# Kernel tuning notes

Measured on AMD Instinct MI355X. Metric: run time of the kernel, lower is better.

The kernel has to match this reference:

```python
import jax, jax.numpy as jnp
import numpy as np

V, H, B, T = 100000, 512, 4096, 524288
EPS = 1e-5

def setup_inputs() -> dict:
    key = jax.random.key(0)
    ks = jax.random.split(key, 8)
    tokens = jax.random.randint(ks[0], (T,), 0, V, dtype=jnp.int32)
    seg_ids = jnp.sort(jax.random.randint(ks[1], (T,), 0, B, dtype=jnp.int32))
    t = jax.random.bernoulli(ks[2], 0.5, (B,)).astype(jnp.float32)
    emb = jax.random.normal(ks[3], (V, H), dtype=jnp.float32) * 0.1
    W1 = jax.random.normal(ks[4], (H, H), dtype=jnp.float32) * (1.0 / np.sqrt(H))
    b1 = jnp.zeros((H,), jnp.float32)
    gamma = jnp.ones((H,), jnp.float32)
    beta = jnp.zeros((H,), jnp.float32)
    w2 = jax.random.normal(ks[5], (H,), dtype=jnp.float32) * (1.0 / np.sqrt(H))
    b2 = jnp.zeros((), jnp.float32)
    return {"tokens": tokens, "seg_ids": seg_ids, "t": t, "emb": emb,
            "W1": W1, "b1": b1, "gamma": gamma, "beta": beta, "w2": w2, "b2": b2}

def reference(tokens, seg_ids, t, emb, W1, b1, gamma, beta, w2, b2):
    nb = t.shape[0]
    # fused gather + segment-mean (bag-of-words), replaces the per-sample loop
    gathered = emb[tokens]  # [T, H]
    sums = jax.ops.segment_sum(gathered, seg_ids, num_segments=nb)  # [B, H]
    counts = jax.ops.segment_sum(jnp.ones((tokens.shape[0],), jnp.float32), seg_ids, num_segments=nb)
    bow = sums / jnp.maximum(counts, 1.0)[:, None]  # [B, H]
    # Linear -> BatchNorm1d (training-mode batch stats, biased var) -> ReLU
    z = bow @ W1.T + b1  # [B, H]
    mu = jnp.mean(z, axis=0)
    var = jnp.mean((z - mu) ** 2, axis=0)
    zn = (z - mu) * jax.lax.rsqrt(var + EPS) * gamma + beta
    h = jax.nn.relu(zn)  # dropout treated as identity (eval mode) for determinism
    logits = h @ w2 + b2  # [B]
    # BCEWithLogitsLoss: mean(softplus(logit) - t*logit), numerically stable
    loss = jnp.mean(jnp.logaddexp(0.0, logits) - t * logits)
    return (loss, logits)
```

## Files before the change

kernel.cpp:

```cpp
#include <hip/hip_runtime.h>
#include <hip/hip_bf16.h>
#include <hip/hip_fp16.h>
#include <math.h>

constexpr int NTOK = 524288;
constexpr int NB   = 4096;
constexpr int H    = 512;
constexpr float EPS = 1e-5f;

typedef _Float16 half8 __attribute__((ext_vector_type(8)));
typedef float f32x4 __attribute__((ext_vector_type(4)));
struct h4 { __half2 a, b; };

__global__ __launch_bounds__(256) void k_convert(
    const float* __restrict__ src, h4* __restrict__ dst) {
  size_t i = (size_t)blockIdx.x * 256 + threadIdx.x;
  float4 v = ((const float4*)src)[i];
  h4 o;
  o.a = __floats2half2_rn(v.x, v.y);
  o.b = __floats2half2_rn(v.z, v.w);
  dst[i] = o;
}

__global__ __launch_bounds__(256) void k_gather_mean(
    const int* __restrict__ tokens, const int* __restrict__ seg,
    const half8* __restrict__ embh, half8* __restrict__ bow_h) {
  const int b = blockIdx.x;
  int lo = 0, hi = NTOK;
  while (lo < hi) { int mid = (lo + hi) >> 1; if (seg[mid] < b) lo = mid + 1; else hi = mid; }
  const int start = lo;
  hi = NTOK;
  while (lo < hi) { int mid = (lo + hi) >> 1; if (seg[mid] < b + 1) lo = mid + 1; else hi = mid; }
  const int end = lo;

  const int tid = threadIdx.x;
  const int lane = tid & 63;
  const int g = tid >> 6;

  float acc[8] = {};
  int i = start + g;
  for (; i + 12 < end; i += 16) {
    half8 v0 = embh[(size_t)tokens[i]      * 64 + lane];
    half8 v1 = embh[(size_t)tokens[i + 4]  * 64 + lane];
    half8 v2 = embh[(size_t)tokens[i + 8]  * 64 + lane];
    half8 v3 = embh[(size_t)tokens[i + 12] * 64 + lane];
#pragma unroll
    for (int j = 0; j < 8; ++j)
      acc[j] += (float)v0[j] + (float)v1[j] + (float)v2[j] + (float)v3[j];
  }
  for (; i < end; i += 4) {
    half8 v0 = embh[(size_t)tokens[i] * 64 + lane];
#pragma unroll
    for (int j = 0; j < 8; ++j) acc[j] += (float)v0[j];
  }

  __shared__ float part[3][64][9];
  if (g > 0) {
#pragma unroll
    for (int j = 0; j < 8; ++j) part[g - 1][lane][j] = acc[j];
  }
  __syncthreads();
  if (g == 0) {
    const int cnt = end - start;
    const float s = 1.0f / (float)(cnt > 0 ? cnt : 1);
    half8 o;
#pragma unroll
    for (int j = 0; j < 8; ++j) {
      float v = acc[j] + part[0][lane][j] + part[1][lane][j] + part[2][lane][j];
      o[j] = (_Float16)(v * s);
    }
    bow_h[(size_t)b * 64 + lane] = o;
  }
}

__global__ __launch_bounds__(256) void k_gemm_mfma(
    const _Float16* __restrict__ A,
    const _Float16* __restrict__ Bw,
    const float* __restrict__ b1, float* __restrict__ C) {
  const int tid = threadIdx.x;
  const int lane = tid & 63;
  const int gw = blockIdx.x * 4 + (tid >> 6);
  const int m0 = (gw >> 3) * 16;
  const int n0 = (gw & 7) * 64;
  const int l15 = lane & 15, quad = lane >> 4;

  f32x4 acc0 = {}, acc1 = {}, acc2 = {}, acc3 = {};
  const _Float16* ap = A + (size_t)(m0 + l15) * H + quad * 8;
  const _Float16* bp = Bw + (size_t)(n0 + l15) * H + quad * 8;

#pragma unroll
  for (int k = 0; k < H; k += 32) {
    half8 af  = *(const half8*)(ap + k);
    half8 bf0 = *(const half8*)(bp + k);
    half8 bf1 = *(const half8*)(bp + 16 * H + k);
    half8 bf2 = *(const half8*)(bp + 32 * H + k);
    half8 bf3 = *(const half8*)(bp + 48 * H + k);
    acc0 = __builtin_amdgcn_mfma_f32_16x16x32_f16(af, bf0, acc0, 0, 0, 0);
    acc1 = __builtin_amdgcn_mfma_f32_16x16x32_f16(af, bf1, acc1, 0, 0, 0);
    acc2 = __builtin_amdgcn_mfma_f32_16x16x32_f16(af, bf2, acc2, 0, 0, 0);
    acc3 = __builtin_amdgcn_mfma_f32_16x16x32_f16(af, bf3, acc3, 0, 0, 0);
  }

  const float bn0v = b1[n0 + l15];
  const float bn1v = b1[n0 + 16 + l15];
  const float bn2v = b1[n0 + 32 + l15];
  const float bn3v = b1[n0 + 48 + l15];
  float* crow = C + (size_t)(m0 + quad * 4) * H + n0 + l15;
#pragma unroll
  for (int r = 0; r < 4; ++r) {
    crow[(size_t)r * H]      = acc0[r] + bn0v;
    crow[(size_t)r * H + 16] = acc1[r] + bn1v;
    crow[(size_t)r * H + 32] = acc2[r] + bn2v;
    crow[(size_t)r * H + 48] = acc3[r] + bn3v;
  }
}

__global__ __launch_bounds__(256) void k_colstats(
    const float* __restrict__ z, float* __restrict__ ps, float* __restrict__ pss) {
  const int blk = blockIdx.x;
  const int c0 = threadIdx.x * 2;
  const int r0 = blk * 64;
  float s0 = 0, s1 = 0, q0 = 0, q1 = 0;
  for (int r = 0; r < 64; ++r) {
    float2 v = *(const float2*)&z[(size_t)(r0 + r) * H + c0];
    s0 += v.x; s1 += v.y;
    q0 += v.x * v.x; q1 += v.y * v.y;
  }
  ps[blk * H + c0] = s0; ps[blk * H + c0 + 1] = s1;
  pss[blk * H + c0] = q0; pss[blk * H + c0 + 1] = q1;
}

__global__ __launch_bounds__(128) void k_finalize(
    const float* __restrict__ ps, const float* __restrict__ pss,
    const float* __restrict__ gamma, const float* __restrict__ beta,
    float* __restrict__ scale, float* __restrict__ shift) {
  const int c = blockIdx.x * 128 + threadIdx.x;
  float s = 0, q = 0;
#pragma unroll 8
  for (int i = 0; i < 64; ++i) { s += ps[i * H + c]; q += pss[i * H + c]; }
  const float mu = s * (1.0f / NB);
  const float var = q * (1.0f / NB) - mu * mu;
  const float rstd = rsqrtf(var + EPS);
  const float sc = rstd * gamma[c];
  scale[c] = sc;
  shift[c] = beta[c] - mu * sc;
}

__global__ __launch_bounds__(256) void k_bn_dot(
    const float* __restrict__ z, const float* __restrict__ scale,
    const float* __restrict__ shift, const float* __restrict__ w2,
    const float* __restrict__ b2, float* __restrict__ out) {
  const int tid = threadIdx.x;
  const int wave = tid >> 6, lane = tid & 63;
  const int b = blockIdx.x * 4 + wave;
  const float4* __restrict__ z4 = (const float4*)(z + (size_t)b * H);
  const float4* __restrict__ sc4 = (const float4*)scale;
  const float4* __restrict__ sh4 = (const float4*)shift;
  const float4* __restrict__ w24 = (const float4*)w2;
  float acc = 0.f;
#pragma unroll
  for (int i = lane; i < 128; i += 64) {
    float4 zv = z4[i], sc = sc4[i], sh = sh4[i], w = w24[i];
    float h0 = fmaxf(zv.x * sc.x + sh.x, 0.f);
    float h1 = fmaxf(zv.y * sc.y + sh.y, 0.f);
    float h2 = fmaxf(zv.z * sc.z + sh.z, 0.f);
    float h3 = fmaxf(zv.w * sc.w + sh.w, 0.f);
    acc += h0 * w.x + h1 * w.y + h2 * w.z + h3 * w.w;
  }
#pragma unroll
  for (int off = 32; off > 0; off >>= 1) acc += __shfl_down(acc, off, 64);
  if (lane == 0) out[1 + b] = acc + b2[0];
}

__global__ __launch_bounds__(1024) void k_loss(
    const float* __restrict__ t, float* __restrict__ d_out) {
  const int tid = threadIdx.x;
  float s = 0.f;
#pragma unroll
  for (int b = tid; b < NB; b += 1024) {
    float x = d_out[1 + b];
    float sp = fmaxf(x, 0.f) + log1pf(expf(-fabsf(x)));
    s += sp - t[b] * x;
  }
  __shared__ float red[1024];
  red[tid] = s;
  __syncthreads();
  for (int off = 512; off > 0; off >>= 1) {
    if (tid < off) red[tid] += red[tid + off];
    __syncthreads();
  }
  if (tid == 0) d_out[0] = red[0] * (1.0f / NB);
}

extern "C" void kernel_launch(void* const* d_in, const int* in_sizes, int n_in,
                              void* d_out, int out_size, void* d_ws, size_t ws_size,
                              hipStream_t stream) {
  const int*   tokens = (const int*)d_in[0];
  const int*   seg    = (const int*)d_in[1];
  const float* t      = (const float*)d_in[2];
  const float* emb    = (const float*)d_in[3];
  const float* W1     = (const float*)d_in[4];
  const float* b1     = (const float*)d_in[5];
  const float* gamma  = (const float*)d_in[6];
  const float* beta   = (const float*)d_in[7];
  const float* w2     = (const float*)d_in[8];
  const float* b2     = (const float*)d_in[9];
  float* out = (float*)d_out;

  char* wsb = (char*)d_ws;
  half8*    embh  = (half8*)wsb;
  _Float16* W1h   = (_Float16*)(wsb + 102400000);
  half8*    bow_h = (half8*)(wsb + 102924288);
  float*    z     = (float*)(wsb + 107118592);
  float*    ps    = (float*)(wsb + 115507200);
  float*    pss   = ps + 64 * H;
  float*    scale = pss + 64 * H;
  float*    shift = scale + H;

  k_convert<<<50000, 256, 0, stream>>>(emb, (h4*)embh);
  k_convert<<<256, 256, 0, stream>>>(W1, (h4*)W1h);
  k_gather_mean<<<NB, 256, 0, stream>>>(tokens, seg, embh, bow_h);
  k_gemm_mfma<<<512, 256, 0, stream>>>((const _Float16*)bow_h, W1h, b1, z);
  k_colstats<<<64, 256, 0, stream>>>(z, ps, pss);
  k_finalize<<<4, 128, 0, stream>>>(ps, pss, gamma, beta, scale, shift);
  k_bn_dot<<<NB / 4, 256, 0, stream>>>(z, scale, shift, w2, b2, out);
  k_loss<<<1, 1024, 0, stream>>>(t, out);
}
```

Before: 420.3 us.

## Precompute segment bounds, unroll gather deeper, fuse loss into BN-dot kernel

```diff
diff --git a/kernel.cpp b/kernel.cpp
--- a/kernel.cpp
+++ b/kernel.cpp
@@ -11,6 +11,17 @@
 typedef _Float16 half8 __attribute__((ext_vector_type(8)));
 typedef float f32x4 __attribute__((ext_vector_type(4)));
 struct h4 { __half2 a, b; };
+
+__global__ __launch_bounds__(256) void k_seg_bounds(
+    const int* __restrict__ seg, int* __restrict__ bounds) {
+  const int i = blockIdx.x * 256 + threadIdx.x;
+  const int s = seg[i];
+  const int sp = (i == 0) ? -1 : seg[i - 1];
+  for (int b = sp + 1; b <= s; ++b) bounds[b] = i;
+  if (i == NTOK - 1) {
+    for (int b = s + 1; b <= NB; ++b) bounds[b] = NTOK;
+  }
+}
 
 __global__ __launch_bounds__(256) void k_convert(
     const float* __restrict__ src, h4* __restrict__ dst) {
@@ -23,15 +34,11 @@
 }
 
 __global__ __launch_bounds__(256) void k_gather_mean(
-    const int* __restrict__ tokens, const int* __restrict__ seg,
+    const int* __restrict__ tokens, const int* __restrict__ bounds,
     const half8* __restrict__ embh, half8* __restrict__ bow_h) {
   const int b = blockIdx.x;
-  int lo = 0, hi = NTOK;
-  while (lo < hi) { int mid = (lo + hi) >> 1; if (seg[mid] < b) lo = mid + 1; else hi = mid; }
-  const int start = lo;
-  hi = NTOK;
-  while (lo < hi) { int mid = (lo + hi) >> 1; if (seg[mid] < b + 1) lo = mid + 1; else hi = mid; }
-  const int end = lo;
+  const int start = bounds[b];
+  const int end   = bounds[b + 1];
 
   const int tid = threadIdx.x;
   const int lane = tid & 63;
@@ -39,14 +46,19 @@
 
   float acc[8] = {};
   int i = start + g;
-  for (; i + 12 < end; i += 16) {
+  for (; i + 28 < end; i += 32) {
     half8 v0 = embh[(size_t)tokens[i]      * 64 + lane];
     half8 v1 = embh[(size_t)tokens[i + 4]  * 64 + lane];
     half8 v2 = embh[(size_t)tokens[i + 8]  * 64 + lane];
     half8 v3 = embh[(size_t)tokens[i + 12] * 64 + lane];
+    half8 v4 = embh[(size_t)tokens[i + 16] * 64 + lane];
+    half8 v5 = embh[(size_t)tokens[i + 20] * 64 + lane];
+    half8 v6 = embh[(size_t)tokens[i + 24] * 64 + lane];
+    half8 v7 = embh[(size_t)tokens[i + 28] * 64 + lane];
 #pragma unroll
     for (int j = 0; j < 8; ++j)
-      acc[j] += (float)v0[j] + (float)v1[j] + (float)v2[j] + (float)v3[j];
+      acc[j] += ((float)v0[j] + (float)v1[j]) + ((float)v2[j] + (float)v3[j]) +
+                ((float)v4[j] + (float)v5[j]) + ((float)v6[j] + (float)v7[j]);
   }
   for (; i < end; i += 4) {
     half8 v0 = embh[(size_t)tokens[i] * 64 + lane];
@@ -133,8 +145,10 @@
 __global__ __launch_bounds__(128) void k_finalize(
     const float* __restrict__ ps, const float* __restrict__ pss,
     const float* __restrict__ gamma, const float* __restrict__ beta,
-    float* __restrict__ scale, float* __restrict__ shift) {
+    float* __restrict__ scale, float* __restrict__ shift,
+    float* __restrict__ d_out) {
   const int c = blockIdx.x * 128 + threadIdx.x;
+  if (c == 0) d_out[0] = 0.f;
   float s = 0, q = 0;
 #pragma unroll 8
   for (int i = 0; i < 64; ++i) { s += ps[i * H + c]; q += pss[i * H + c]; }
@@ -146,10 +160,11 @@
   shift[c] = beta[c] - mu * sc;
 }
 
-__global__ __launch_bounds__(256) void k_bn_dot(
+__global__ __launch_bounds__(256) void k_bn_dot_loss(
     const float* __restrict__ z, const float* __restrict__ scale,
     const float* __restrict__ shift, const float* __restrict__ w2,
-    const float* __restrict__ b2, float* __restrict__ out) {
+    const float* __restrict__ b2, const float* __restrict__ t,
+    float* __restrict__ out) {
   const int tid = threadIdx.x;
   const int wave = tid >> 6, lane = tid & 63;
   const int b = blockIdx.x * 4 + wave;
@@ -169,27 +184,19 @@
   }
 #pragma unroll
   for (int off = 32; off > 0; off >>= 1) acc += __shfl_down(acc, off, 64);
-  if (lane == 0) out[1 + b] = acc + b2[0];
-}
-
-__global__ __launch_bounds__(1024) void k_loss(
-    const float* __restrict__ t, float* __restrict__ d_out) {
-  const int tid = threadIdx.x;
-  float s = 0.f;
-#pragma unroll
-  for (int b = tid; b < NB; b += 1024) {
-    float x = d_out[1 + b];
-    float sp = fmaxf(x, 0.f) + log1pf(expf(-fabsf(x)));
-    s += sp - t[b] * x;
-  }
-  __shared__ float red[1024];
-  red[tid] = s;
+
+  __shared__ float lred[4];
+  if (lane == 0) {
+    const float x = acc + b2[0];
+    out[1 + b] = x;
+    const float sp = fmaxf(x, 0.f) + log1pf(expf(-fabsf(x)));
+    lred[wave] = sp - t[b] * x;
+  }
   __syncthreads();
-  for (int off = 512; off > 0; off >>= 1) {
-    if (tid < off) red[tid] += red[tid + off];
-    __syncthreads();
-  }
-  if (tid == 0) d_out[0] = red[0] * (1.0f / NB);
+  if (tid == 0) {
+    const float ls = (lred[0] + lred[1] + lred[2] + lred[3]) * (1.0f / NB);
+    atomicAdd(out, ls);
+  }
 }
 
 extern "C" void kernel_launch(void* const* d_in, const int* in_sizes, int n_in,
@@ -208,21 +215,22 @@
   float* out = (float*)d_out;
 
   char* wsb = (char*)d_ws;
-  half8*    embh  = (half8*)wsb;
-  _Float16* W1h   = (_Float16*)(wsb + 102400000);
-  half8*    bow_h = (half8*)(wsb + 102924288);
-  float*    z     = (float*)(wsb + 107118592);
-  float*    ps    = (float*)(wsb + 115507200);
-  float*    pss   = ps + 64 * H;
-  float*    scale = pss + 64 * H;
-  float*    shift = scale + H;
-
+  half8*    embh   = (half8*)wsb;
+  _Float16* W1h    = (_Float16*)(wsb + 102400000);
+  half8*    bow_h  = (half8*)(wsb + 102924288);
+  float*    z      = (float*)(wsb + 107118592);
+  float*    ps     = (float*)(wsb + 115507200);
+  float*    pss    = ps + 64 * H;
+  float*    scale  = pss + 64 * H;
+  float*    shift  = scale + H;
+  int*      bounds = (int*)(shift + H);
+
+  k_seg_bounds<<<NTOK / 256, 256, 0, stream>>>(seg, bounds);
   k_convert<<<50000, 256, 0, stream>>>(emb, (h4*)embh);
   k_convert<<<256, 256, 0, stream>>>(W1, (h4*)W1h);
-  k_gather_mean<<<NB, 256, 0, stream>>>(tokens, seg, embh, bow_h);
+  k_gather_mean<<<NB, 256, 0, stream>>>(tokens, bounds, embh, bow_h);
   k_gemm_mfma<<<512, 256, 0, stream>>>((const _Float16*)bow_h, W1h, b1, z);
   k_colstats<<<64, 256, 0, stream>>>(z, ps, pss);
-  k_finalize<<<4, 128, 0, stream>>>(ps, pss, gamma, beta, scale, shift);
-  k_bn_dot<<<NB / 4, 256, 0, stream>>>(z, scale, shift, w2, b2, out);
-  k_loss<<<1, 1024, 0, stream>>>(t, out);
-}
+  k_finalize<<<4, 128, 0, stream>>>(ps, pss, gamma, beta, scale, shift, out);
+  k_bn_dot_loss<<<NB / 4, 256, 0, stream>>>(z, scale, shift, w2, b2, t, out);
+}
```

After: 420.5 us. Within noise of the previous version (+0.1%).
